# Performance work log

Measured on AMD Instinct MI355X. Metric: run time of the kernel, lower is better.

Reference implementation:

```python
import jax, jax.numpy as jnp
import numpy as np


def _gru_dirs(x, h, w_ih, w_hh, b_ih, b_hh):
    # One GRU step for both directions at once (seq_len==1 per original loop).
    # x: [N, in], h: [2, N, H]; w_ih: [2, 3H, in], w_hh: [2, 3H, H], biases [2, 3H]
    gi = jnp.einsum('ni,dgi->dng', x, w_ih) + b_ih[:, None, :]
    gh = jnp.einsum('dnh,dgh->dng', h, w_hh) + b_hh[:, None, :]
    H = h.shape[-1]
    ir, iz, inn = gi[..., :H], gi[..., H:2 * H], gi[..., 2 * H:]
    hr, hz, hn = gh[..., :H], gh[..., H:2 * H], gh[..., 2 * H:]
    r = jax.nn.sigmoid(ir + hr)
    z = jax.nn.sigmoid(iz + hz)
    n = jnp.tanh(inn + r * hn)
    return (1.0 - z) * n + z * h


def setup_inputs() -> dict:
    key = jax.random.key(0)
    ks = jax.random.split(key, 6)
    V, E, H, NL = 32000, 1024, 512, 2  # vocab, input_size, hidden_size, num_layers
    N, L = 32, 512
    s = 0.05
    x = jax.random.randint(ks[0], (N, L), 0, V)
    emb = jax.random.normal(ks[1], (V, E), dtype=jnp.float32) * s
    w_ih = jax.random.normal(ks[2], (NL, 2, 3 * H, E), dtype=jnp.float32) * s
    w_hh = jax.random.normal(ks[3], (NL, 2, 3 * H, H), dtype=jnp.float32) * s
    b_ih = jax.random.normal(ks[4], (NL, 2, 3 * H), dtype=jnp.float32) * s
    b_hh = jax.random.normal(ks[5], (NL, 2, 3 * H), dtype=jnp.float32) * s
    return {"x": x, "emb": emb, "w_ih": w_ih, "w_hh": w_hh, "b_ih": b_ih, "b_hh": b_hh}


def reference(x, emb, w_ih, w_hh, b_ih, b_hh):
    # Because the torch code calls the bidirectional GRU one timestep at a time
    # with a carried hidden, BOTH directions scan left-to-right over the sequence.
    N, L = x.shape
    num_layers = w_ih.shape[0]
    H = w_hh.shape[-1]
    h0 = jnp.zeros((num_layers, 2, N, H), dtype=emb.dtype)

    def step(h, xt):
        layer_in = emb[xt]  # [N, E] embedding lookup for this timestep
        new_h = []
        for l in range(num_layers):  # fixed small layer loop
            hl = _gru_dirs(layer_in, h[l], w_ih[l], w_hh[l], b_ih[l], b_hh[l])
            new_h.append(hl)
            layer_in = jnp.concatenate([hl[0], hl[1]], axis=-1)  # [N, 2H]
        hs = jnp.stack(new_h)  # [num_layers, 2, N, H]
        return hs, (layer_in, hs)

    _, (outs, hiddens) = jax.lax.scan(step, h0, x.T)  # scan over L timesteps
    outputs = jnp.transpose(outs, (1, 0, 2))  # [N, L, 2H]
    hiddens = hiddens.reshape(L, num_layers * 2, N, H)  # [L, 2*num_layers, N, H]
    return outputs, hiddens
```

## Files before the change

### kernel.cpp

```cpp
#include <hip/hip_runtime.h>
#include <hip/hip_bf16.h>

using u16 = unsigned short;
using u32 = unsigned int;
using bf16x8 = __attribute__((ext_vector_type(8))) __bf16;
using f32x4  = __attribute__((ext_vector_type(4))) float;
using u32x4  = __attribute__((ext_vector_type(4))) u32;

#define GLP(p) ((const __attribute__((address_space(1))) void*)(p))
#define LDSP(p) ((__attribute__((address_space(3))) void*)(p))

__device__ __forceinline__ float bf2f(u16 u) {
    union { float f; u32 i; } v; v.i = ((u32)u) << 16; return v.f;
}
__device__ __forceinline__ u16 f2bf(float f) {
    union { float f; u32 i; } v; v.f = f;
    u32 r = v.i + 0x7FFFu + ((v.i >> 16) & 1u);
    return (u16)(r >> 16);
}

__device__ __forceinline__ u32 ld_sc01_u32(const u32* p) {
    u32 v;
    asm volatile("global_load_dword %0, %1, off sc0 sc1\n\ts_waitcnt vmcnt(0)"
                 : "=v"(v) : "v"(p) : "memory");
    return v;
}
__device__ __forceinline__ void st_sc01_u32(u32* p, u32 v) {
    asm volatile("global_store_dword %0, %1, off sc0 sc1" :: "v"(p), "v"(v) : "memory");
}
__device__ __forceinline__ void st_sc01_u16(u16* p, u16 v) {
    asm volatile("global_store_short %0, %1, off sc0 sc1" :: "v"(p), "v"(v) : "memory");
}
__device__ __forceinline__ void st_sc01_u32x4(u16* p, u32x4 v) {
    asm volatile("global_store_dwordx4 %0, %1, off sc0 sc1" :: "v"(p), "v"(v) : "memory");
}

__global__ void k_gather(const int* __restrict__ x, const float* __restrict__ emb,
                         u16* __restrict__ X0) {
    int gid = blockIdx.x * blockDim.x + threadIdx.x;
    if (gid >= 16384 * 256) return;
    int e4 = gid << 2;
    int m = e4 >> 10, k = e4 & 1023;
    int t = m >> 5, n = m & 31;
    int tok = x[n * 512 + t];
    float4 v = *reinterpret_cast<const float4*>(emb + ((size_t)tok << 10) + k);
    ushort4 o;
    o.x = f2bf(v.x); o.y = f2bf(v.y); o.z = f2bf(v.z); o.w = f2bf(v.w);
    *reinterpret_cast<ushort4*>(X0 + (size_t)e4) = o;
}

__global__ void k_f32bf16(const float* __restrict__ s, u16* __restrict__ d, int n4) {
    int gid = blockIdx.x * blockDim.x + threadIdx.x;
    if (gid >= n4) return;
    float4 v = reinterpret_cast<const float4*>(s)[gid];
    ushort4 o;
    o.x = f2bf(v.x); o.y = f2bf(v.y); o.z = f2bf(v.z); o.w = f2bf(v.w);
    reinterpret_cast<ushort4*>(d)[gid] = o;
}

__global__ __launch_bounds__(256) void k_gemm(const u16* __restrict__ A,
                                              const u16* __restrict__ B,
                                              const float* __restrict__ bias,
                                              u16* __restrict__ C,
                                              int M, int N, int K) {
    __shared__ __align__(16) u16 As[128 * 64];
    __shared__ __align__(16) u16 Bs[128 * 64];
    const int tid = threadIdx.x;
    const int lane = tid & 63, wid = tid >> 6;
    const int wm = wid >> 1, wn = wid & 1;
    const int m0 = blockIdx.y * 128, n0 = blockIdx.x * 128;
    const int lr = lane & 15, lk = lane >> 4;
    f32x4 zero = {0.f, 0.f, 0.f, 0.f};
    f32x4 acc[4][4];
    #pragma unroll
    for (int i = 0; i < 4; ++i)
        #pragma unroll
        for (int j = 0; j < 4; ++j) acc[i][j] = zero;

    for (int k0 = 0; k0 < K; k0 += 64) {
        #pragma unroll
        for (int r = 0; r < 4; ++r) {
            int c = wid * 4 + r;
            int o = c * 1024 + lane * 16;
            int row = o >> 7;
            int kb = o & 127;
            int kbs = kb ^ ((row & 7) << 4);
            const char* sa = (const char*)A + ((size_t)(m0 + row) * K + k0) * 2 + kbs;
            const char* sb = (const char*)B + ((size_t)(n0 + row) * K + k0) * 2 + kbs;
            __builtin_amdgcn_global_load_lds(GLP(sa), LDSP((char*)As + c * 1024), 16, 0, 0);
            __builtin_amdgcn_global_load_lds(GLP(sb), LDSP((char*)Bs + c * 1024), 16, 0, 0);
        }
        __syncthreads();
        #pragma unroll
        for (int kk = 0; kk < 2; ++kk) {
            bf16x8 af[4], bfr[4];
            #pragma unroll
            for (int i = 0; i < 4; ++i) {
                int rowA = wm * 64 + i * 16 + lr;
                int rowB = wn * 64 + i * 16 + lr;
                int kb = kk * 64 + lk * 16;
                af[i]  = *reinterpret_cast<const bf16x8*>((const char*)As + rowA * 128 + (kb ^ ((rowA & 7) << 4)));
                bfr[i] = *reinterpret_cast<const bf16x8*>((const char*)Bs + rowB * 128 + (kb ^ ((rowB & 7) << 4)));
            }
            #pragma unroll
            for (int i = 0; i < 4; ++i)
                #pragma unroll
                for (int j = 0; j < 4; ++j)
                    acc[i][j] = __builtin_amdgcn_mfma_f32_16x16x32_bf16(af[i], bfr[j], acc[i][j], 0, 0, 0);
        }
        __syncthreads();
    }
    #pragma unroll
    for (int j = 0; j < 4; ++j) {
        int col = n0 + wn * 64 + j * 16 + lr;
        float bv = bias[col];
        #pragma unroll
        for (int i = 0; i < 4; ++i) {
            int rowb = m0 + wm * 64 + i * 16 + lk * 4;
            #pragma unroll
            for (int q = 0; q < 4; ++q)
                C[(size_t)(rowb + q) * N + col] = f2bf(acc[i][j][q] + bv);
        }
    }
}

template<int LAYER>
__device__ __forceinline__ void gru_body(char* smem, int d, int wg,
    const u16* __restrict__ Gi, const u16* __restrict__ Whh_l,
    const float* __restrict__ bhh_l, u16* __restrict__ hbuf,
    u16* __restrict__ X1, float* __restrict__ hid, float* __restrict__ outp,
    u32* __restrict__ flags, u32* __restrict__ xflags, const u32* __restrict__ gdone)
{
    char* hS          = smem;
    float (*ghs)[196] = (float(*)[196])(smem + 32768);
    u16 (*gis)[208]   = (u16(*)[208])(smem + 57856);
    float* bhh_s      = (float*)(smem + 71168);
    u16* hvS          = (u16*)(smem + 71936);
    const int tid = threadIdx.x;
    const int lane = tid & 63, w = tid >> 6;
    const int j0 = wg * 64;
    const int g = w >> 2, joff = (w & 3) * 16;
    const int lr = lane & 15, lk = lane >> 4;

    if (tid < 192) {
        int g2 = tid >> 6, jj = tid & 63;
        bhh_s[tid] = bhh_l[d * 1536 + g2 * 512 + j0 + jj];
    }
    bf16x8 wf[16];
    {
        const u16* wr = Whh_l + (size_t)(d * 1536 + g * 512 + j0 + joff + lr) * 512 + lk * 8;
        #pragma unroll
        for (int kt = 0; kt < 16; ++kt)
            wf[kt] = *reinterpret_cast<const bf16x8*>(wr + kt * 32);
    }
    if (LAYER == 1 && tid == 0) {
        long long T0 = __builtin_amdgcn_s_memrealtime();
        while (ld_sc01_u32(&gdone[0]) == 0) {
            __builtin_amdgcn_s_sleep(4);
            if (__builtin_amdgcn_s_memrealtime() - T0 > 2000000) break;
        }
    }
    __syncthreads();

    const int p_nb = tid / 24, p_gc = tid % 24;
    const int p_lg = p_gc * 8;
    const int p_col = d * 1536 + (p_lg >> 6) * 512 + j0 + (p_lg & 63);
    const u32* myflags = flags + d * 8 * 32;
    u32* myflag  = flags  + (d * 8 + wg) * 32;
    u32* myxflag = (LAYER == 0) ? xflags + (d * 8 + wg) * 32 : nullptr;

    const int srow = tid >> 6;
    const int scol = (tid & 63) * 8;
    const int scb  = (tid & 63) * 16;

    float hp0 = 0.f, hp1 = 0.f, hp2 = 0.f;
    uint4 gv;
    if (LAYER == 0)
        gv = *reinterpret_cast<const uint4*>(Gi + (size_t)p_nb * 3072 + p_col);

    for (int t = 0; t < 512; ++t) {
        if (t > 0) {
            if (tid < 8) {
                const u32* fp = myflags + tid * 32;
                long long tt0 = __builtin_amdgcn_s_memrealtime();
                while (ld_sc01_u32(fp) < (u32)t) {
                    __builtin_amdgcn_s_sleep(1);
                    if (__builtin_amdgcn_s_memrealtime() - tt0 > 2000) {
                        __hip_atomic_store(myflag, (u32)t, __ATOMIC_RELEASE,
                                           __HIP_MEMORY_SCOPE_AGENT);
                        tt0 = __builtin_amdgcn_s_memrealtime();
                    }
                }
            } else if (LAYER == 1 && tid == 8) {
                long long tt0 = __builtin_amdgcn_s_memrealtime();
                while (ld_sc01_u32(&gdone[t >> 2]) == 0) {
                    __builtin_amdgcn_s_sleep(1);
                    if (__builtin_amdgcn_s_memrealtime() - tt0 > 2000000) break;
                }
            }
            __syncthreads();
        }

        const u16* hb = hbuf + ((size_t)d * 2 + ((t + 1) & 1)) * 16384;
        u32x4 va0, va1, vb0, vb1, gvv;
        if (tid < 512) {
            asm volatile("global_load_dwordx4 %0, %1, off sc0 sc1"
                         : "=v"(va0) : "v"(hb + (size_t)srow * 512 + scol));
            asm volatile("global_load_dwordx4 %0, %1, off sc0 sc1"
                         : "=v"(va1) : "v"(hb + (size_t)(srow + 8) * 512 + scol));
            asm volatile("global_load_dwordx4 %0, %1, off sc0 sc1"
                         : "=v"(vb0) : "v"(hb + (size_t)(srow + 16) * 512 + scol));
            asm volatile("global_load_dwordx4 %0, %1, off sc0 sc1"
                         : "=v"(vb1) : "v"(hb + (size_t)(srow + 24) * 512 + scol));
        }
        if (LAYER == 1) {
            const u16* gip = Gi + (size_t)(t * 32 + p_nb) * 3072 + p_col;
            asm volatile("global_load_dwordx4 %0, %1, off sc0 sc1" : "=v"(gvv) : "v"(gip));
        }
        if (tid < 512) {
            if (LAYER == 0) asm volatile("s_waitcnt vmcnt(2)" ::: "memory");
            else            asm volatile("s_waitcnt vmcnt(3)" ::: "memory");
            int r0 = srow, r1 = srow + 8;
            *reinterpret_cast<u32x4*>(hS + r0 * 1024 + (scb ^ ((r0 & 15) << 4))) = va0;
            *reinterpret_cast<u32x4*>(hS + r1 * 1024 + (scb ^ ((r1 & 15) << 4))) = va1;
        }
        __syncthreads();

        f32x4 acc0 = {0.f, 0.f, 0.f, 0.f};
        #pragma unroll
        for (int kt = 0; kt < 16; ++kt) {
            int boff = (lk * 16 + kt * 64) ^ (lr << 4);
            bf16x8 a = *reinterpret_cast<const bf16x8*>(hS + lr * 1024 + boff);
            acc0 = __builtin_amdgcn_mfma_f32_16x16x32_bf16(a, wf[kt], acc0, 0, 0, 0);
        }
        if (tid < 512) {
            asm volatile("s_waitcnt vmcnt(0)" ::: "memory");
            int r2 = srow + 16, r3 = srow + 24;
            *reinterpret_cast<u32x4*>(hS + r2 * 1024 + (scb ^ ((r2 & 15) << 4))) = vb0;
            *reinterpret_cast<u32x4*>(hS + r3 * 1024 + (scb ^ ((r3 & 15) << 4))) = vb1;
        } else if (LAYER == 1) {
            asm volatile("s_waitcnt vmcnt(0)" ::: "memory");
        }
        if (LAYER == 0) {
            *reinterpret_cast<uint4*>(&gis[p_nb][p_lg]) = gv;
        } else {
            *reinterpret_cast<u32x4*>(&gis[p_nb][p_lg]) = gvv;
        }
        __syncthreads();

        f32x4 acc1 = {0.f, 0.f, 0.f, 0.f};
        #pragma unroll
        for (int kt = 0; kt < 16; ++kt) {
            int boff = (lk * 16 + kt * 64) ^ (lr << 4);
            bf16x8 a = *reinterpret_cast<const bf16x8*>(hS + (16 + lr) * 1024 + boff);
            acc1 = __builtin_amdgcn_mfma_f32_16x16x32_bf16(a, wf[kt], acc1, 0, 0, 0);
        }
        int colg = w * 16 + lr;
        float bv = bhh_s[colg];
        #pragma unroll
        for (int q = 0; q < 4; ++q) {
            ghs[lk * 4 + q][colg]      = acc0[q] + bv;
            ghs[16 + lk * 4 + q][colg] = acc1[q] + bv;
        }
        if (LAYER == 0) {
            int tn = (t + 1 < 512) ? t + 1 : t;
            gv = *reinterpret_cast<const uint4*>(Gi + (size_t)(tn * 32 + p_nb) * 3072 + p_col);
        }
        __syncthreads();

        u16* hbw = hbuf + ((size_t)d * 2 + (t & 1)) * 16384;
        #pragma unroll
        for (int rep = 0; rep < 3; ++rep) {
            int e = tid + rep * 768;
            if (e < 2048) {
                int j = e & 63, nb = e >> 6;
                float gr = bf2f(gis[nb][j])       + ghs[nb][j];
                float gz = bf2f(gis[nb][64 + j])  + ghs[nb][64 + j];
                float r = 1.f / (1.f + __expf(-gr));
                float z = 1.f / (1.f + __expf(-gz));
                float ng = tanhf(bf2f(gis[nb][128 + j]) + r * ghs[nb][128 + j]);
                float hp = (rep == 0) ? hp0 : (rep == 1) ? hp1 : hp2;
                float hv = (1.f - z) * ng + z * hp;
                if (rep == 0) hp0 = hv; else if (rep == 1) hp1 = hv; else hp2 = hv;
                u16 hb16 = f2bf(hv);
                st_sc01_u16(hbw + (size_t)nb * 512 + j0 + j, hb16);
                hvS[nb * 64 + j] = hb16;
            }
        }
        asm volatile("s_waitcnt vmcnt(0)" ::: "memory");
        __syncthreads();
        if (tid == 16)
            st_sc01_u32(myflag, (u32)(t + 1));

        if (tid >= 512) {
            int q = tid - 512, nb = q >> 3, j8 = (q & 7) * 8;
            union { u32x4 v; u16 s[8]; } h8;
            h8.v = *reinterpret_cast<const u32x4*>(hvS + nb * 64 + j8);
            float f0 = bf2f(h8.s[0]), f1 = bf2f(h8.s[1]), f2 = bf2f(h8.s[2]), f3 = bf2f(h8.s[3]);
            float f4 = bf2f(h8.s[4]), f5 = bf2f(h8.s[5]), f6 = bf2f(h8.s[6]), f7 = bf2f(h8.s[7]);
            float* hp = hid + ((size_t)(t * 4 + LAYER * 2 + d) * 32 + nb) * 512 + j0 + j8;
            *reinterpret_cast<float4*>(hp)     = make_float4(f0, f1, f2, f3);
            *reinterpret_cast<float4*>(hp + 4) = make_float4(f4, f5, f6, f7);
            if (LAYER == 0) {
                u16* xp = X1 + (size_t)(t * 32 + nb) * 1024 + (size_t)d * 512 + j0 + j8;
                st_sc01_u32x4(xp, h8.v);
            } else {
                float* op = outp + ((size_t)nb * 512 + t) * 1024 + (size_t)d * 512 + j0 + j8;
                *reinterpret_cast<float4*>(op)     = make_float4(f0, f1, f2, f3);
                *reinterpret_cast<float4*>(op + 4) = make_float4(f4, f5, f6, f7);
            }
        }
        if (LAYER == 0 && (t & 3) == 3) {
            asm volatile("s_waitcnt vmcnt(0)" ::: "memory");
            __syncthreads();
            if (tid == 17)
                st_sc01_u32(myxflag, (u32)(t + 1));
        }
    }
}

__device__ __forceinline__ void chaser_body(char* smem, int w,
    const u16* __restrict__ X1, const u16* __restrict__ Wih1,
    const float* __restrict__ bih1, u16* __restrict__ Gi,
    const u32* __restrict__ xflags, u32* __restrict__ cnt, u32* __restrict__ gdone)
{
    u16* As = (u16*)smem;
    u16* Bs = (u16*)(smem + 16384);
    const int tid = threadIdx.x;
    const int lane = tid & 63, wid = tid >> 6;
    const int wm = wid & 1, wn = wid >> 1;
    const int lr = lane & 15, lk = lane >> 4;
    const int x = w & 31, yg = w >> 5;

    for (int y = yg; y < 128; y += 3) {
        if (tid < 16) {
            const u32* fp = xflags + tid * 32;
            u32 target = 4u * (u32)y + 4u;
            long long T0 = __builtin_amdgcn_s_memrealtime();
            while (ld_sc01_u32(fp) < target) {
                __builtin_amdgcn_s_sleep(4);
                if (__builtin_amdgcn_s_memrealtime() - T0 > 2000000) break;
            }
        }
        __syncthreads();

        f32x4 zero = {0.f, 0.f, 0.f, 0.f};
        f32x4 acc[4][2];
        #pragma unroll
        for (int i = 0; i < 4; ++i) { acc[i][0] = zero; acc[i][1] = zero; }

        for (int k0 = 0; k0 < 1024; k0 += 64) {
            #pragma unroll
            for (int r = 0; r < 5; ++r) {
                int c = wid * 5 + r;
                if (c < 16) {
                    int o = c * 1024 + lane * 16;
                    int row = o >> 7, kb = o & 127;
                    int kbs = kb ^ ((row & 7) << 4);
                    const char* s = (const char*)X1 + ((size_t)(y * 128 + row) * 1024 + k0) * 2 + kbs;
                    __builtin_amdgcn_global_load_lds(GLP(s), LDSP((char*)As + c * 1024), 16, 0, 0);
                } else if (c < 28) {
                    int c2 = c - 16;
                    int o = c2 * 1024 + lane * 16;
                    int row = o >> 7, kb = o & 127;
                    int kbs = kb ^ ((row & 7) << 4);
                    const char* s = (const char*)Wih1 + ((size_t)(x * 96 + row) * 1024 + k0) * 2 + kbs;
                    __builtin_amdgcn_global_load_lds(GLP(s), LDSP((char*)Bs + c2 * 1024), 16, 0, 0);
                }
            }
            __syncthreads();
            if (wid < 6) {
                #pragma unroll
                for (int kk = 0; kk < 2; ++kk) {
                    bf16x8 af[4], bfr[2];
                    int kb = kk * 64 + lk * 16;
                    #pragma unroll
                    for (int i = 0; i < 4; ++i) {
                        int rowA = wm * 64 + i * 16 + lr;
                        af[i] = *reinterpret_cast<const bf16x8*>((const char*)As + rowA * 128 + (kb ^ ((rowA & 7) << 4)));
                    }
                    #pragma unroll
                    for (int j = 0; j < 2; ++j) {
                        int rowB = wn * 32 + j * 16 + lr;
                        bfr[j] = *reinterpret_cast<const bf16x8*>((const char*)Bs + rowB * 128 + (kb ^ ((rowB & 7) << 4)));
                    }
                    #pragma unroll
                    for (int i = 0; i < 4; ++i)
                        #pragma unroll
                        for (int j = 0; j < 2; ++j)
                            acc[i][j] = __builtin_amdgcn_mfma_f32_16x16x32_bf16(af[i], bfr[j], acc[i][j], 0, 0, 0);
                }
            }
            __syncthreads();
        }
        if (wid < 6) {
            #pragma unroll
            for (int j = 0; j < 2; ++j) {
                int col = x * 96 + wn * 32 + j * 16 + lr;
                float bv = bih1[col];
                #pragma unroll
                for (int i = 0; i < 4; ++i) {
                    int rowb = y * 128 + wm * 64 + i * 16 + lk * 4;
                    #pragma unroll
                    for (int q = 0; q < 4; ++q)
                        st_sc01_u16(Gi + (size_t)(rowb + q) * 3072 + col, f2bf(acc[i][j][q] + bv));
                }
            }
        }
        asm volatile("s_waitcnt vmcnt(0)" ::: "memory");
        __syncthreads();
        if (tid == 0) {
            u32 old = __hip_atomic_fetch_add(&cnt[y], 1u, __ATOMIC_RELAXED,
                                             __HIP_MEMORY_SCOPE_AGENT);
            if (old == 31u)
                st_sc01_u32(&gdone[y], 1u);
        }
    }
}

__global__ __launch_bounds__(768, 3) void k_fused(
    const u16* __restrict__ Gi_r, u16* __restrict__ Gi_w,
    const u16* __restrict__ Whh, const float* __restrict__ bhh,
    u16* __restrict__ hbuf0, u16* __restrict__ hbuf1,
    u16* __restrict__ X1, const u16* __restrict__ Wih1, const float* __restrict__ bih1,
    float* __restrict__ hid, float* __restrict__ outp,
    u32* __restrict__ flags0, u32* __restrict__ flags1,
    u32* __restrict__ xflags, u32* __restrict__ cnt, u32* __restrict__ gdone)
{
    __shared__ __align__(16) char smem[76032];
    int bid = blockIdx.x;
    if (bid < 16) {
        gru_body<0>(smem, bid >> 3, bid & 7, Gi_r, Whh, bhh, hbuf0,
                    X1, hid, outp, flags0, xflags, nullptr);
    } else if (bid < 112) {
        chaser_body(smem, bid - 16, X1, Wih1, bih1, Gi_w, xflags, cnt, gdone);
    } else {
        int b = bid - 112;
        gru_body<1>(smem, b >> 3, b & 7, Gi_r, Whh + (size_t)3072 * 512, bhh + 3072,
                    hbuf1, nullptr, hid, outp, flags1, nullptr, gdone);
    }
}

extern "C" void kernel_launch(void* const* d_in, const int* in_sizes, int n_in,
                              void* d_out, int out_size, void* d_ws, size_t ws_size,
                              hipStream_t stream) {
    const int*   x    = (const int*)d_in[0];
    const float* emb  = (const float*)d_in[1];
    const float* w_ih = (const float*)d_in[2];
    const float* w_hh = (const float*)d_in[3];
    const float* b_ih = (const float*)d_in[4];
    const float* b_hh = (const float*)d_in[5];
    float* outp = (float*)d_out;
    float* hid  = outp + (size_t)32 * 512 * 1024;

    char* ws = (char*)d_ws;
    u16* X0     = (u16*)(ws);
    u16* X1     = (u16*)(ws + 33554432);
    u16* Wih    = (u16*)(ws + 67108864);
    u16* Whh    = (u16*)(ws + 79691776);
    u16* Gi     = (u16*)(ws + 85983232);
    u16* hbuf0  = (u16*)(ws + 186646528);
    u16* hbuf1  = (u16*)(ws + 186777600);
    u32* flags0 = (u32*)(ws + 186908672);
    u32* flags1 = (u32*)(ws + 186910720);
    u32* xflags = (u32*)(ws + 186912768);
    u32* cnt    = (u32*)(ws + 186914816);
    u32* gdone  = (u32*)(ws + 186915328);

    k_gather<<<16384, 256, 0, stream>>>(x, emb, X0);
    k_f32bf16<<<(1572864 + 255) / 256, 256, 0, stream>>>(w_ih, Wih, 1572864);
    k_f32bf16<<<( 786432 + 255) / 256, 256, 0, stream>>>(w_hh, Whh, 786432);

    (void)hipMemsetAsync(hbuf0, 0, 269312, stream);

    k_gemm<<<dim3(24, 128), 256, 0, stream>>>(X0, Wih, b_ih, Gi, 16384, 3072, 1024);

    k_fused<<<128, 768, 0, stream>>>(Gi, Gi, Whh, b_hh, hbuf0, hbuf1,
                                     X1, Wih + (size_t)3072 * 1024, b_ih + 3072,
                                     hid, outp, flags0, flags1, xflags, cnt, gdone);
}
```

Measured before the change: 2.271 ms.

## Fuse layer-0 input GEMM into persistent kernel with chaser blocks

The standalone layer-0 input-projection GEMM is removed. Its work moves into the persistent fused kernel, where 48 chaser blocks compute Gi tiles and publish per-row-block done flags, so the layer-0 recurrence can start before the whole GEMM finishes. The GRU step is also restructured: waves 0-7 each poll one peer flag and stage h, waves 8-11 wait on gdone and stage Gi, and the two MFMA passes are merged into one loop. This trades the separate GEMM launch and its serial latency for chaser blocks sharing the GPU with the latency-bound recurrence, and it halves the chaser count available to layer 1.

Measured after the change: 2.141 ms, median of 2. 5.7% less time.

```diff
diff --git a/kernel.cpp b/kernel.cpp
--- a/kernel.cpp
+++ b/kernel.cpp
@@ -56,72 +56,6 @@
     ushort4 o;
     o.x = f2bf(v.x); o.y = f2bf(v.y); o.z = f2bf(v.z); o.w = f2bf(v.w);
     reinterpret_cast<ushort4*>(d)[gid] = o;
-}
-
-__global__ __launch_bounds__(256) void k_gemm(const u16* __restrict__ A,
-                                              const u16* __restrict__ B,
-                                              const float* __restrict__ bias,
-                                              u16* __restrict__ C,
-                                              int M, int N, int K) {
-    __shared__ __align__(16) u16 As[128 * 64];
-    __shared__ __align__(16) u16 Bs[128 * 64];
-    const int tid = threadIdx.x;
-    const int lane = tid & 63, wid = tid >> 6;
-    const int wm = wid >> 1, wn = wid & 1;
-    const int m0 = blockIdx.y * 128, n0 = blockIdx.x * 128;
-    const int lr = lane & 15, lk = lane >> 4;
-    f32x4 zero = {0.f, 0.f, 0.f, 0.f};
-    f32x4 acc[4][4];
-    #pragma unroll
-    for (int i = 0; i < 4; ++i)
-        #pragma unroll
-        for (int j = 0; j < 4; ++j) acc[i][j] = zero;
-
-    for (int k0 = 0; k0 < K; k0 += 64) {
-        #pragma unroll
-        for (int r = 0; r < 4; ++r) {
-            int c = wid * 4 + r;
-            int o = c * 1024 + lane * 16;
-            int row = o >> 7;
-            int kb = o & 127;
-            int kbs = kb ^ ((row & 7) << 4);
-            const char* sa = (const char*)A + ((size_t)(m0 + row) * K + k0) * 2 + kbs;
-            const char* sb = (const char*)B + ((size_t)(n0 + row) * K + k0) * 2 + kbs;
-            __builtin_amdgcn_global_load_lds(GLP(sa), LDSP((char*)As + c * 1024), 16, 0, 0);
-            __builtin_amdgcn_global_load_lds(GLP(sb), LDSP((char*)Bs + c * 1024), 16, 0, 0);
-        }
-        __syncthreads();
-        #pragma unroll
-        for (int kk = 0; kk < 2; ++kk) {
-            bf16x8 af[4], bfr[4];
-            #pragma unroll
-            for (int i = 0; i < 4; ++i) {
-                int rowA = wm * 64 + i * 16 + lr;
-                int rowB = wn * 64 + i * 16 + lr;
-                int kb = kk * 64 + lk * 16;
-                af[i]  = *reinterpret_cast<const bf16x8*>((const char*)As + rowA * 128 + (kb ^ ((rowA & 7) << 4)));
-                bfr[i] = *reinterpret_cast<const bf16x8*>((const char*)Bs + rowB * 128 + (kb ^ ((rowB & 7) << 4)));
-            }
-            #pragma unroll
-            for (int i = 0; i < 4; ++i)
-                #pragma unroll
-                for (int j = 0; j < 4; ++j)
-                    acc[i][j] = __builtin_amdgcn_mfma_f32_16x16x32_bf16(af[i], bfr[j], acc[i][j], 0, 0, 0);
-        }
-        __syncthreads();
-    }
-    #pragma unroll
-    for (int j = 0; j < 4; ++j) {
-        int col = n0 + wn * 64 + j * 16 + lr;
-        float bv = bias[col];
-        #pragma unroll
-        for (int i = 0; i < 4; ++i) {
-            int rowb = m0 + wm * 64 + i * 16 + lk * 4;
-            #pragma unroll
-            for (int q = 0; q < 4; ++q)
-                C[(size_t)(rowb + q) * N + col] = f2bf(acc[i][j][q] + bv);
-        }
-    }
 }
 
 template<int LAYER>
@@ -139,7 +73,7 @@
     const int tid = threadIdx.x;
     const int lane = tid & 63, w = tid >> 6;
     const int j0 = wg * 64;
-    const int g = w >> 2, joff = (w & 3) * 16;
+    const int g = w >> 2;
     const int lr = lane & 15, lk = lane >> 4;
 
     if (tid < 192) {
@@ -148,112 +82,93 @@
     }
     bf16x8 wf[16];
     {
+        const int joff = (w & 3) * 16;
         const u16* wr = Whh_l + (size_t)(d * 1536 + g * 512 + j0 + joff + lr) * 512 + lk * 8;
         #pragma unroll
         for (int kt = 0; kt < 16; ++kt)
             wf[kt] = *reinterpret_cast<const bf16x8*>(wr + kt * 32);
     }
-    if (LAYER == 1 && tid == 0) {
-        long long T0 = __builtin_amdgcn_s_memrealtime();
-        while (ld_sc01_u32(&gdone[0]) == 0) {
-            __builtin_amdgcn_s_sleep(4);
-            if (__builtin_amdgcn_s_memrealtime() - T0 > 2000000) break;
-        }
-    }
     __syncthreads();
 
-    const int p_nb = tid / 24, p_gc = tid % 24;
-    const int p_lg = p_gc * 8;
-    const int p_col = d * 1536 + (p_lg >> 6) * 512 + j0 + (p_lg & 63);
-    const u32* myflags = flags + d * 8 * 32;
-    u32* myflag  = flags  + (d * 8 + wg) * 32;
+    u32* myflag = flags + (d * 8 + wg) * 32;
+    const u32* wflag = flags + (d * 8 + (w & 7)) * 32;
     u32* myxflag = (LAYER == 0) ? xflags + (d * 8 + wg) * 32 : nullptr;
 
-    const int srow = tid >> 6;
-    const int scol = (tid & 63) * 8;
-    const int scb  = (tid & 63) * 16;
+    const int c8 = (lane & 7) * 8;
+    const int rb = lane >> 3;
+    const int colu = w * 64 + c8;
+    const int ci0 = (tid - 512) * 3;
 
     float hp0 = 0.f, hp1 = 0.f, hp2 = 0.f;
-    uint4 gv;
-    if (LAYER == 0)
-        gv = *reinterpret_cast<const uint4*>(Gi + (size_t)p_nb * 3072 + p_col);
+    u32 g_seen = 0;
 
     for (int t = 0; t < 512; ++t) {
-        if (t > 0) {
-            if (tid < 8) {
-                const u32* fp = myflags + tid * 32;
+        if (w < 8) {
+            if (t > 0) {
                 long long tt0 = __builtin_amdgcn_s_memrealtime();
-                while (ld_sc01_u32(fp) < (u32)t) {
+                while (ld_sc01_u32(wflag) < (u32)t) {
                     __builtin_amdgcn_s_sleep(1);
                     if (__builtin_amdgcn_s_memrealtime() - tt0 > 2000) {
-                        __hip_atomic_store(myflag, (u32)t, __ATOMIC_RELEASE,
-                                           __HIP_MEMORY_SCOPE_AGENT);
+                        if (lane == 0)
+                            __hip_atomic_store(myflag, (u32)t, __ATOMIC_RELEASE,
+                                               __HIP_MEMORY_SCOPE_AGENT);
                         tt0 = __builtin_amdgcn_s_memrealtime();
                     }
                 }
-            } else if (LAYER == 1 && tid == 8) {
-                long long tt0 = __builtin_amdgcn_s_memrealtime();
-                while (ld_sc01_u32(&gdone[t >> 2]) == 0) {
+            }
+            const u16* hb = hbuf + ((size_t)d * 2 + ((t + 1) & 1)) * 16384;
+            u32x4 v0, v1, v2, v3;
+            asm volatile("global_load_dwordx4 %0, %1, off sc0 sc1"
+                         : "=v"(v0) : "v"(hb + (size_t)(rb)      * 512 + colu));
+            asm volatile("global_load_dwordx4 %0, %1, off sc0 sc1"
+                         : "=v"(v1) : "v"(hb + (size_t)(rb + 8)  * 512 + colu));
+            asm volatile("global_load_dwordx4 %0, %1, off sc0 sc1"
+                         : "=v"(v2) : "v"(hb + (size_t)(rb + 16) * 512 + colu));
+            asm volatile("global_load_dwordx4 %0, %1, off sc0 sc1"
+                         : "=v"(v3) : "v"(hb + (size_t)(rb + 24) * 512 + colu));
+            asm volatile("s_waitcnt vmcnt(0)" ::: "memory");
+            const int cb = colu * 2;
+            *reinterpret_cast<u32x4*>(hS + (rb)      * 1024 + (cb ^ (((rb)      & 15) << 4))) = v0;
+            *reinterpret_cast<u32x4*>(hS + (rb + 8)  * 1024 + (cb ^ (((rb + 8)  & 15) << 4))) = v1;
+            *reinterpret_cast<u32x4*>(hS + (rb + 16) * 1024 + (cb ^ (((rb + 16) & 15) << 4))) = v2;
+            *reinterpret_cast<u32x4*>(hS + (rb + 24) * 1024 + (cb ^ (((rb + 24) & 15) << 4))) = v3;
+        } else {
+            u32 yneed = (u32)(t >> 2);
+            if (g_seen <= yneed) {
+                const u32* gp = gdone + yneed;
+                long long T0 = __builtin_amdgcn_s_memrealtime();
+                while (ld_sc01_u32(gp) == 0) {
                     __builtin_amdgcn_s_sleep(1);
-                    if (__builtin_amdgcn_s_memrealtime() - tt0 > 2000000) break;
+                    if (__builtin_amdgcn_s_memrealtime() - T0 > 2000000) break;
                 }
-            }
-            __syncthreads();
-        }
-
-        const u16* hb = hbuf + ((size_t)d * 2 + ((t + 1) & 1)) * 16384;
-        u32x4 va0, va1, vb0, vb1, gvv;
-        if (tid < 512) {
-            asm volatile("global_load_dwordx4 %0, %1, off sc0 sc1"
-                         : "=v"(va0) : "v"(hb + (size_t)srow * 512 + scol));
-            asm volatile("global_load_dwordx4 %0, %1, off sc0 sc1"
-                         : "=v"(va1) : "v"(hb + (size_t)(srow + 8) * 512 + scol));
-            asm volatile("global_load_dwordx4 %0, %1, off sc0 sc1"
-                         : "=v"(vb0) : "v"(hb + (size_t)(srow + 16) * 512 + scol));
-            asm volatile("global_load_dwordx4 %0, %1, off sc0 sc1"
-                         : "=v"(vb1) : "v"(hb + (size_t)(srow + 24) * 512 + scol));
-        }
-        if (LAYER == 1) {
-            const u16* gip = Gi + (size_t)(t * 32 + p_nb) * 3072 + p_col;
-            asm volatile("global_load_dwordx4 %0, %1, off sc0 sc1" : "=v"(gvv) : "v"(gip));
-        }
-        if (tid < 512) {
-            if (LAYER == 0) asm volatile("s_waitcnt vmcnt(2)" ::: "memory");
-            else            asm volatile("s_waitcnt vmcnt(3)" ::: "memory");
-            int r0 = srow, r1 = srow + 8;
-            *reinterpret_cast<u32x4*>(hS + r0 * 1024 + (scb ^ ((r0 & 15) << 4))) = va0;
-            *reinterpret_cast<u32x4*>(hS + r1 * 1024 + (scb ^ ((r1 & 15) << 4))) = va1;
+                g_seen = yneed + 1;
+            }
+            u32x4 gq[3];
+            int nbs[3], gcs[3];
+            #pragma unroll
+            for (int i = 0; i < 3; ++i) {
+                int ci = ci0 + i;
+                nbs[i] = ci / 24; gcs[i] = ci % 24;
+                const u16* gp = Gi + (size_t)(t * 32 + nbs[i]) * 3072 + d * 1536
+                              + (gcs[i] >> 3) * 512 + j0 + (gcs[i] & 7) * 8;
+                asm volatile("global_load_dwordx4 %0, %1, off sc0 sc1"
+                             : "=v"(gq[i]) : "v"(gp));
+            }
+            asm volatile("s_waitcnt vmcnt(0)" ::: "memory");
+            #pragma unroll
+            for (int i = 0; i < 3; ++i)
+                *reinterpret_cast<u32x4*>(&gis[nbs[i]][gcs[i] * 8]) = gq[i];
         }
         __syncthreads();
 
-        f32x4 acc0 = {0.f, 0.f, 0.f, 0.f};
+        f32x4 acc0 = {0.f, 0.f, 0.f, 0.f}, acc1 = acc0;
         #pragma unroll
         for (int kt = 0; kt < 16; ++kt) {
             int boff = (lk * 16 + kt * 64) ^ (lr << 4);
-            bf16x8 a = *reinterpret_cast<const bf16x8*>(hS + lr * 1024 + boff);
-            acc0 = __builtin_amdgcn_mfma_f32_16x16x32_bf16(a, wf[kt], acc0, 0, 0, 0);
-        }
-        if (tid < 512) {
-            asm volatile("s_waitcnt vmcnt(0)" ::: "memory");
-            int r2 = srow + 16, r3 = srow + 24;
-            *reinterpret_cast<u32x4*>(hS + r2 * 1024 + (scb ^ ((r2 & 15) << 4))) = vb0;
-            *reinterpret_cast<u32x4*>(hS + r3 * 1024 + (scb ^ ((r3 & 15) << 4))) = vb1;
-        } else if (LAYER == 1) {
-            asm volatile("s_waitcnt vmcnt(0)" ::: "memory");
-        }
-        if (LAYER == 0) {
-            *reinterpret_cast<uint4*>(&gis[p_nb][p_lg]) = gv;
-        } else {
-            *reinterpret_cast<u32x4*>(&gis[p_nb][p_lg]) = gvv;
-        }
-        __syncthreads();
-
-        f32x4 acc1 = {0.f, 0.f, 0.f, 0.f};
-        #pragma unroll
-        for (int kt = 0; kt < 16; ++kt) {
-            int boff = (lk * 16 + kt * 64) ^ (lr << 4);
-            bf16x8 a = *reinterpret_cast<const bf16x8*>(hS + (16 + lr) * 1024 + boff);
-            acc1 = __builtin_amdgcn_mfma_f32_16x16x32_bf16(a, wf[kt], acc1, 0, 0, 0);
+            bf16x8 a0 = *reinterpret_cast<const bf16x8*>(hS + lr * 1024 + boff);
+            bf16x8 a1 = *reinterpret_cast<const bf16x8*>(hS + (16 + lr) * 1024 + boff);
+            acc0 = __builtin_amdgcn_mfma_f32_16x16x32_bf16(a0, wf[kt], acc0, 0, 0, 0);
+            acc1 = __builtin_amdgcn_mfma_f32_16x16x32_bf16(a1, wf[kt], acc1, 0, 0, 0);
         }
         int colg = w * 16 + lr;
         float bv = bhh_s[colg];
@@ -261,10 +176,6 @@
         for (int q = 0; q < 4; ++q) {
             ghs[lk * 4 + q][colg]      = acc0[q] + bv;
             ghs[16 + lk * 4 + q][colg] = acc1[q] + bv;
-        }
-        if (LAYER == 0) {
-            int tn = (t + 1 < 512) ? t + 1 : t;
-            gv = *reinterpret_cast<const uint4*>(Gi + (size_t)(tn * 32 + p_nb) * 3072 + p_col);
         }
         __syncthreads();
 
@@ -319,10 +230,10 @@
     }
 }
 
-__device__ __forceinline__ void chaser_body(char* smem, int w,
-    const u16* __restrict__ X1, const u16* __restrict__ Wih1,
-    const float* __restrict__ bih1, u16* __restrict__ Gi,
-    const u32* __restrict__ xflags, u32* __restrict__ cnt, u32* __restrict__ gdone)
+__device__ __forceinline__ void chaser_body(char* smem, int cw,
+    const u16* __restrict__ A, const u16* __restrict__ B,
+    const float* __restrict__ bias, u16* __restrict__ Gi,
+    const u32* __restrict__ xflags, u32* __restrict__ cnt, u32* __restrict__ done)
 {
     u16* As = (u16*)smem;
     u16* Bs = (u16*)(smem + 16384);
@@ -330,10 +241,10 @@
     const int lane = tid & 63, wid = tid >> 6;
     const int wm = wid & 1, wn = wid >> 1;
     const int lr = lane & 15, lk = lane >> 4;
-    const int x = w & 31, yg = w >> 5;
-
-    for (int y = yg; y < 128; y += 3) {
-        if (tid < 16) {
+
+    for (int T = cw; T < 4096; T += 48) {
+        const int y = T >> 5, x = T & 31;
+        if (xflags && tid < 16) {
             const u32* fp = xflags + tid * 32;
             u32 target = 4u * (u32)y + 4u;
             long long T0 = __builtin_amdgcn_s_memrealtime();
@@ -357,14 +268,14 @@
                     int o = c * 1024 + lane * 16;
                     int row = o >> 7, kb = o & 127;
                     int kbs = kb ^ ((row & 7) << 4);
-                    const char* s = (const char*)X1 + ((size_t)(y * 128 + row) * 1024 + k0) * 2 + kbs;
+                    const char* s = (const char*)A + ((size_t)(y * 128 + row) * 1024 + k0) * 2 + kbs;
                     __builtin_amdgcn_global_load_lds(GLP(s), LDSP((char*)As + c * 1024), 16, 0, 0);
                 } else if (c < 28) {
                     int c2 = c - 16;
                     int o = c2 * 1024 + lane * 16;
                     int row = o >> 7, kb = o & 127;
                     int kbs = kb ^ ((row & 7) << 4);
-                    const char* s = (const char*)Wih1 + ((size_t)(x * 96 + row) * 1024 + k0) * 2 + kbs;
+                    const char* s = (const char*)B + ((size_t)(x * 96 + row) * 1024 + k0) * 2 + kbs;
                     __builtin_amdgcn_global_load_lds(GLP(s), LDSP((char*)Bs + c2 * 1024), 16, 0, 0);
                 }
             }
@@ -397,7 +308,7 @@
             #pragma unroll
             for (int j = 0; j < 2; ++j) {
                 int col = x * 96 + wn * 32 + j * 16 + lr;
-                float bv = bih1[col];
+                float bv = bias[col];
                 #pragma unroll
                 for (int i = 0; i < 4; ++i) {
                     int rowb = y * 128 + wm * 64 + i * 16 + lk * 4;
@@ -413,31 +324,38 @@
             u32 old = __hip_atomic_fetch_add(&cnt[y], 1u, __ATOMIC_RELAXED,
                                              __HIP_MEMORY_SCOPE_AGENT);
             if (old == 31u)
-                st_sc01_u32(&gdone[y], 1u);
+                st_sc01_u32((u32*)&done[y], 1u);
         }
     }
 }
 
-__global__ __launch_bounds__(768, 3) void k_fused(
-    const u16* __restrict__ Gi_r, u16* __restrict__ Gi_w,
+__global__ __launch_bounds__(768, 2) void k_fused(
+    u16* __restrict__ Gi,
+    const u16* __restrict__ X0, const u16* __restrict__ Wih,
+    const float* __restrict__ b_ih,
     const u16* __restrict__ Whh, const float* __restrict__ bhh,
     u16* __restrict__ hbuf0, u16* __restrict__ hbuf1,
-    u16* __restrict__ X1, const u16* __restrict__ Wih1, const float* __restrict__ bih1,
+    u16* __restrict__ X1,
     float* __restrict__ hid, float* __restrict__ outp,
     u32* __restrict__ flags0, u32* __restrict__ flags1,
-    u32* __restrict__ xflags, u32* __restrict__ cnt, u32* __restrict__ gdone)
+    u32* __restrict__ xflags,
+    u32* __restrict__ g0cnt, u32* __restrict__ g0done,
+    u32* __restrict__ g1cnt, u32* __restrict__ g1done)
 {
     __shared__ __align__(16) char smem[76032];
     int bid = blockIdx.x;
     if (bid < 16) {
-        gru_body<0>(smem, bid >> 3, bid & 7, Gi_r, Whh, bhh, hbuf0,
-                    X1, hid, outp, flags0, xflags, nullptr);
+        gru_body<0>(smem, bid >> 3, bid & 7, Gi, Whh, bhh, hbuf0,
+                    X1, hid, outp, flags0, xflags, g0done);
+    } else if (bid < 64) {
+        chaser_body(smem, bid - 16, X0, Wih, b_ih, Gi, nullptr, g0cnt, g0done);
     } else if (bid < 112) {
-        chaser_body(smem, bid - 16, X1, Wih1, bih1, Gi_w, xflags, cnt, gdone);
+        chaser_body(smem, bid - 64, X1, Wih + (size_t)3072 * 1024, b_ih + 3072,
+                    Gi, xflags, g1cnt, g1done);
     } else {
         int b = bid - 112;
-        gru_body<1>(smem, b >> 3, b & 7, Gi_r, Whh + (size_t)3072 * 512, bhh + 3072,
-                    hbuf1, nullptr, hid, outp, flags1, nullptr, gdone);
+        gru_body<1>(smem, b >> 3, b & 7, Gi, Whh + (size_t)3072 * 512, bhh + 3072,
+                    hbuf1, nullptr, hid, outp, flags1, nullptr, g1done);
     }
 }
 
@@ -464,18 +382,19 @@
     u32* flags0 = (u32*)(ws + 186908672);
     u32* flags1 = (u32*)(ws + 186910720);
     u32* xflags = (u32*)(ws + 186912768);
-    u32* cnt    = (u32*)(ws + 186914816);
-    u32* gdone  = (u32*)(ws + 186915328);
+    u32* g0cnt  = (u32*)(ws + 186914816);
+    u32* g0done = (u32*)(ws + 186915328);
+    u32* g1cnt  = (u32*)(ws + 186915840);
+    u32* g1done = (u32*)(ws + 186916352);
 
     k_gather<<<16384, 256, 0, stream>>>(x, emb, X0);
     k_f32bf16<<<(1572864 + 255) / 256, 256, 0, stream>>>(w_ih, Wih, 1572864);
     k_f32bf16<<<( 786432 + 255) / 256, 256, 0, stream>>>(w_hh, Whh, 786432);
 
-    (void)hipMemsetAsync(hbuf0, 0, 269312, stream);
-
-    k_gemm<<<dim3(24, 128), 256, 0, stream>>>(X0, Wih, b_ih, Gi, 16384, 3072, 1024);
-
-    k_fused<<<128, 768, 0, stream>>>(Gi, Gi, Whh, b_hh, hbuf0, hbuf1,
-                                     X1, Wih + (size_t)3072 * 1024, b_ih + 3072,
-                                     hid, outp, flags0, flags1, xflags, cnt, gdone);
-}
+    (void)hipMemsetAsync(hbuf0, 0, 270336, stream);
+
+    k_fused<<<128, 768, 0, stream>>>(Gi, X0, Wih, b_ih, Whh, b_hh,
+                                     hbuf0, hbuf1, X1, hid, outp,
+                                     flags0, flags1, xflags,
+                                     g0cnt, g0done, g1cnt, g1done);
+}
```
